# Kernel optimization log

Measured on AMD Instinct MI355X. Metric: run time of the kernel, lower is better.

## Reference

```python
import jax, jax.numpy as jnp
import numpy as np

BUCKET_SIZE = 64
N_HASHES = 8
SELF_ATTN_VALUE = -5e4  # TOKEN_SELF_ATTN_VALUE
EPS = 1e-12  # F.normalize eps


def setup_inputs() -> dict:
    key = jax.random.key(0)
    k1, k2, k3 = jax.random.split(key, 3)
    B, S, D = 16, 4096, 128
    n_buckets = S // BUCKET_SIZE  # 64
    qk = jax.random.normal(k1, (B, S, D), dtype=jnp.float32)
    v = jax.random.normal(k2, (B, S, D), dtype=jnp.float32)
    # rotations_shape = (1, dim, n_hashes, n_buckets // 2); shared across batch
    rotations = jax.random.normal(k3, (1, D, N_HASHES, n_buckets // 2), dtype=jnp.float32)
    return {"qk": qk, "v": v, "rotations": rotations}


def _hash_vectors(qk, rotations, n_buckets):
    # qk: (B,S,D), rotations: (1,D,H,n_buckets//2)
    rotated = jnp.einsum('btf,fhi->bhti', qk, rotations[0])  # (B,H,S,nb/2)
    rotated = jnp.concatenate([rotated, -rotated], axis=-1)   # (B,H,S,nb)
    buckets = jnp.argmax(rotated, axis=-1)                    # (B,H,S)
    offsets = (jnp.arange(N_HASHES) * n_buckets)[None, :, None]
    return (buckets + offsets).reshape(qk.shape[0], -1)       # (B, H*S)


def _look_one_back(x):
    # concat each chunk with its predecessor (circular), along the window dim
    return jnp.concatenate([x, jnp.roll(x, 1, axis=1)], axis=2)


def reference(qk, v, rotations):
    B, S, D = qk.shape
    H = N_HASHES
    n_buckets = S // BUCKET_SIZE
    buckets = _hash_vectors(qk, rotations, n_buckets)         # (B, H*S) int

    ticker = jnp.broadcast_to(jnp.arange(H * S)[None, :], (B, H * S))
    buckets_and_t = S * buckets + (ticker % S)                # unique keys
    sticker = jnp.argsort(buckets_and_t, axis=-1)             # sort by bucket
    undo_sort = jnp.argsort(sticker, axis=-1)

    st = sticker % S                                          # original positions
    sqk = jnp.take_along_axis(qk, st[..., None], axis=1)      # (B,H*S,D)
    sv = jnp.take_along_axis(v, st[..., None], axis=1)

    C = H * n_buckets                                         # num chunks
    bq_t = st.reshape(B, C, -1)                               # (B,C,w)
    bqk = sqk.reshape(B, C, -1, D)
    bv = sv.reshape(B, C, -1, D)
    bq = bqk
    nrm = jnp.maximum(jnp.linalg.norm(bqk, axis=-1, keepdims=True), EPS)
    bk = bqk / nrm                                            # F.normalize

    bk = _look_one_back(bk)                                   # (B,C,2w,D)
    bv = _look_one_back(bv)
    bkv_t = _look_one_back(bq_t)                              # (B,C,2w)

    dots = jnp.einsum('bcie,bcje->bcij', bq, bk) * (D ** -0.5)  # (B,C,w,2w)
    self_mask = bq_t[:, :, :, None] == bkv_t[:, :, None, :]
    dots = jnp.where(self_mask, SELF_ATTN_VALUE, dots)

    lse = jax.scipy.special.logsumexp(dots, axis=-1, keepdims=True)
    probs = jnp.exp(dots - lse)
    bo = jnp.einsum('bcij,bcje->bcie', probs, bv)             # (B,C,w,D)

    so = bo.reshape(B, -1, D)                                 # (B,H*S,D)
    slogits = lse.reshape(B, -1)                              # (B,H*S)
    o = jnp.take_along_axis(so, undo_sort[..., None], axis=1)
    logits = jnp.take_along_axis(slogits, undo_sort, axis=1)

    o = o.reshape(B, H, S, D)
    logits = logits.reshape(B, H, S, 1)
    w = jnp.exp(logits - jax.scipy.special.logsumexp(logits, axis=1, keepdims=True))
    out = jnp.sum(o * w, axis=1)                              # (B,S,D)
    return out
```

## Files before the change

kernel.cpp:

```cpp
#include <hip/hip_runtime.h>
#include <hip/hip_bf16.h>


#define B_ 16
#define S_ 4096
#define D_ 128
#define H_ 8
#define C_ 512
#define L_ 8
#define SCALE_ 0.08838834764831845f

typedef __attribute__((ext_vector_type(8))) short bf16x8;
typedef __attribute__((ext_vector_type(8))) _Float16 f16x8;
typedef __attribute__((ext_vector_type(2))) _Float16 f16x2t;
typedef __attribute__((ext_vector_type(4))) float f32x4;
typedef __attribute__((ext_vector_type(2))) float f32x2v;
typedef __attribute__((ext_vector_type(4))) int int4v;

union BF8U { int4v i; bf16x8 b; };
union F16x8U { int4v i; f16x8 h; };

__device__ __forceinline__ unsigned hi_pack(float x0, float x1) {
    unsigned a, b;
    __builtin_memcpy(&b, &x0, 4);
    __builtin_memcpy(&a, &x1, 4);
    return __builtin_amdgcn_perm(a, b, 0x07060302u);
}
__device__ __forceinline__ float truncbf(float x) {
    unsigned u; __builtin_memcpy(&u, &x, 4);
    u &= 0xFFFF0000u;
    float f; __builtin_memcpy(&f, &u, 4);
    return f;
}
__device__ __forceinline__ unsigned pack2f16(float x0, float x1) {
    f16x2t h = {(_Float16)x0, (_Float16)x1};
    unsigned u; __builtin_memcpy(&u, &h, 4);
    return u;
}
__device__ __forceinline__ unsigned enc_ks(unsigned u) {
    return (u & 0x80000000u) ? ~u : (u | 0x80000000u);
}
__device__ __forceinline__ float dec_ks(unsigned ks) {
    unsigned u = (ks & 0x80000000u) ? (ks ^ 0x80000000u) : ~ks;
    float f; __builtin_memcpy(&f, &u, 4);
    return f;
}

__global__ __launch_bounds__(256) void norm_kernel(const float* __restrict__ qk,
                                                   float* __restrict__ rnrm) {
    int half = threadIdx.x >> 5;
    int lane32 = threadIdx.x & 31;
    size_t row = (size_t)blockIdx.x * 8 + half;
    float4 vv = ((const float4*)(qk + row * D_))[lane32];
    float ss = vv.x * vv.x + vv.y * vv.y + vv.z * vv.z + vv.w * vv.w;
    #pragma unroll
    for (int m = 1; m < 32; m <<= 1) ss += __shfl_xor(ss, m, 64);
    if (lane32 == 0) rnrm[row] = 1.0f / fmaxf(sqrtf(ss), 1e-12f);
}

__global__ __launch_bounds__(256) void prep_rot_kernel(const float* __restrict__ rot,
                                                       short* __restrict__ rth,
                                                       short* __restrict__ rtl) {
    int x = blockIdx.x * 256 + threadIdx.x;
    int hp = x >> 11;
    int ia = (x >> 5) & 63;
    int ft = x & 31;
    float v0 = rot[(size_t)(ft * 4 + 0) * 256 + hp * 64 + ia];
    float v1 = rot[(size_t)(ft * 4 + 1) * 256 + hp * 64 + ia];
    float v2 = rot[(size_t)(ft * 4 + 2) * 256 + hp * 64 + ia];
    float v3 = rot[(size_t)(ft * 4 + 3) * 256 + hp * 64 + ia];
    unsigned h0 = hi_pack(v0, v1), h1 = hi_pack(v2, v3);
    unsigned l0 = hi_pack(v0 - truncbf(v0), v1 - truncbf(v1));
    unsigned l1 = hi_pack(v2 - truncbf(v2), v3 - truncbf(v3));
    int off = ia * 128 + ((((ft >> 1) ^ (ia & 7)) << 3) | ((ft & 1) << 2));
    *(int2*)&rth[hp * 8192 + off] = make_int2((int)h0, (int)h1);
    *(int2*)&rtl[hp * 8192 + off] = make_int2((int)l0, (int)l1);
}

__global__ __launch_bounds__(256, 4) void hash_kernel(
        const float* __restrict__ qk, const float* __restrict__ rot,
        const short* __restrict__ rth, const short* __restrict__ rtl,
        int* __restrict__ buckets) {
    __shared__ unsigned char flags[2][64];

    const int bid = blockIdx.x;
    const int b = bid >> 8;
    const int tile = (bid >> 2) & 63;
    const int hp = bid & 3;
    const int tid = threadIdx.x;
    const int w = tid >> 6, l = tid & 63, g = l >> 4, m = l & 15;

    if (tid < 8) ((int4*)flags)[tid] = make_int4(0, 0, 0, 0);
    __syncthreads();

    const float* qrow = qk + ((size_t)b * S_ + (size_t)tile * 64 + w * 16 + m) * D_;
    bf16x8 qh[4], qlr[4];
    #pragma unroll
    for (int s = 0; s < 4; ++s) {
        float4 xa = *(const float4*)(qrow + s * 32 + g * 8);
        float4 xb = *(const float4*)(qrow + s * 32 + g * 8 + 4);
        BF8U hu, lu;
        hu.i[0] = (int)hi_pack(xa.x, xa.y); hu.i[1] = (int)hi_pack(xa.z, xa.w);
        hu.i[2] = (int)hi_pack(xb.x, xb.y); hu.i[3] = (int)hi_pack(xb.z, xb.w);
        lu.i[0] = (int)hi_pack(xa.x - truncbf(xa.x), xa.y - truncbf(xa.y));
        lu.i[1] = (int)hi_pack(xa.z - truncbf(xa.z), xa.w - truncbf(xa.w));
        lu.i[2] = (int)hi_pack(xb.x - truncbf(xb.x), xb.y - truncbf(xb.y));
        lu.i[3] = (int)hi_pack(xb.z - truncbf(xb.z), xb.w - truncbf(xb.w));
        qh[s] = hu.b; qlr[s] = lu.b;
    }

    f32x4 dots_n[4];
    #pragma unroll
    for (int nt = 0; nt < 4; ++nt) {
        f32x4 acc = (f32x4){0.f, 0.f, 0.f, 0.f};
        #pragma unroll
        for (int s = 0; s < 4; ++s) {
            int kr = hp * 8192 + (nt * 16 + m) * 128 + (((s * 4 + g) ^ (m & 7)) << 3);
            bf16x8 bh = *(const bf16x8*)&rth[kr];
            bf16x8 bl = *(const bf16x8*)&rtl[kr];
            acc = __builtin_amdgcn_mfma_f32_16x16x32_bf16(qh[s], bh, acc, 0, 0, 0);
            acc = __builtin_amdgcn_mfma_f32_16x16x32_bf16(qh[s], bl, acc, 0, 0, 0);
            acc = __builtin_amdgcn_mfma_f32_16x16x32_bf16(qlr[s], bh, acc, 0, 0, 0);
            acc = __builtin_amdgcn_mfma_f32_16x16x32_bf16(qlr[s], bl, acc, 0, 0, 0);
        }
        dots_n[nt] = acc;
    }

    #pragma unroll
    for (int hh = 0; hh < 2; ++hh) {
        int h = hp * 2 + hh;
        #pragma unroll
        for (int r = 0; r < 4; ++r) {
            unsigned long long kM = 0ull, kS = 0ull;
            #pragma unroll
            for (int nn = 0; nn < 2; ++nn) {
                float v = dots_n[hh * 2 + nn][r];
                unsigned u; __builtin_memcpy(&u, &v, 4);
                int i = nn * 16 + m;
                unsigned long long kp =
                    ((unsigned long long)enc_ks(u) << 6) | (unsigned)(63 - i);
                unsigned long long kn =
                    ((unsigned long long)enc_ks(u ^ 0x80000000u) << 6) |
                    (unsigned)(63 - (i + 32));
                if (kp > kM) { kS = kM; kM = kp; } else if (kp > kS) kS = kp;
                if (kn > kM) { kS = kM; kM = kn; } else if (kn > kS) kS = kn;
            }
            #pragma unroll
            for (int st = 1; st <= 8; st <<= 1) {
                unsigned long long oM = __shfl_xor(kM, st, 64);
                unsigned long long oS = __shfl_xor(kS, st, 64);
                unsigned long long lo = kM < oM ? kM : oM;
                kM = kM > oM ? kM : oM;
                unsigned long long hs = kS > oS ? kS : oS;
                kS = hs > lo ? hs : lo;
            }
            if (m == 0) {
                int tok = w * 16 + g * 4 + r;
                int i1 = 63 - (int)(kM & 63ull);
                float v1 = dec_ks((unsigned)(kM >> 6));
                float v2 = dec_ks((unsigned)(kS >> 6));
                if (v1 - v2 < 1e-3f) flags[hh][tok] = 1;
                buckets[(((size_t)(b * H_ + h)) << 12) + tile * 64 + tok] = i1;
            }
        }
    }
    __syncthreads();

    int tok = tid >> 2, part = tid & 3;
    const float* qtok = qk + ((size_t)b * S_ + (size_t)tile * 64 + tok) * D_;
    for (int hh = 0; hh < 2; ++hh) {
        if (!flags[hh][tok]) continue;
        int h = hp * 2 + hh;
        double pd[8] = {0, 0, 0, 0, 0, 0, 0, 0};
        #pragma unroll 2
        for (int f = 0; f < 128; ++f) {
            double q = (double)qtok[f];
            const float* rp = rot + (size_t)f * 256 + h * 32 + part * 8;
            float4 r0 = *(const float4*)rp;
            float4 r1 = *(const float4*)(rp + 4);
            pd[0] = fma(q, (double)r0.x, pd[0]);
            pd[1] = fma(q, (double)r0.y, pd[1]);
            pd[2] = fma(q, (double)r0.z, pd[2]);
            pd[3] = fma(q, (double)r0.w, pd[3]);
            pd[4] = fma(q, (double)r1.x, pd[4]);
            pd[5] = fma(q, (double)r1.y, pd[5]);
            pd[6] = fma(q, (double)r1.z, pd[6]);
            pd[7] = fma(q, (double)r1.w, pd[7]);
        }
        double bv = -1e300; int bi = 0;
        #pragma unroll
        for (int ii = 0; ii < 8; ++ii) {
            int i = part * 8 + ii;
            double v = pd[ii];
            if (v > bv || (v == bv && i < bi)) { bv = v; bi = i; }
            double nv = -v; int ni = i + 32;
            if (nv > bv || (nv == bv && ni < bi)) { bv = nv; bi = ni; }
        }
        #pragma unroll
        for (int mm = 1; mm <= 2; mm <<= 1) {
            double ov = __shfl_xor(bv, mm, 64);
            int oi = __shfl_xor(bi, mm, 64);
            if (ov > bv || (ov == bv && oi < bi)) { bv = ov; bi = oi; }
        }
        if (part == 0)
            buckets[(((size_t)(b * H_ + h)) << 12) + tile * 64 + tok] = bi;
    }
}

__global__ __launch_bounds__(256) void sort_kernel(const int* __restrict__ buckets,
                                                   int* __restrict__ st,
                                                   int* __restrict__ inv,
                                                   const float* __restrict__ rnrm,
                                                   float* __restrict__ rnrm_s) {
    __shared__ unsigned short hist[256][64];
    __shared__ int base[64];
    __shared__ int totals[64];
    int tid = threadIdx.x;
    const int* bkrow = buckets + (size_t)blockIdx.x * S_;
    const float* rnb = rnrm + (size_t)(blockIdx.x >> 3) * S_;

    unsigned int* h32 = (unsigned int*)hist;
    #pragma unroll
    for (int u = 0; u < 32; ++u) h32[u * 256 + tid] = 0;
    __syncthreads();

    #pragma unroll
    for (int u = 0; u < 16; ++u) {
        int t = tid * 16 + u;
        int bk = bkrow[t];
        hist[tid][bk]++;
    }
    __syncthreads();

    if (tid < 64) {
        int bucket = tid;
        int run = 0;
        for (int ch = 0; ch < 256; ++ch) {
            int v = hist[ch][bucket];
            hist[ch][bucket] = (unsigned short)run;
            run += v;
        }
        totals[bucket] = run;
    }
    __syncthreads();
    if (tid == 0) {
        int acc = 0;
        for (int k = 0; k < 64; ++k) { base[k] = acc; acc += totals[k]; }
    }
    __syncthreads();

    int* strow = st + (size_t)blockIdx.x * S_;
    int* invrow = inv + (size_t)blockIdx.x * S_;
    float* rnsrow = rnrm_s + (size_t)blockIdx.x * S_;
    #pragma unroll
    for (int u = 0; u < 16; ++u) {
        int t = tid * 16 + u;
        int bk = bkrow[t];
        int off = hist[tid][bk];
        hist[tid][bk] = (unsigned short)(off + 1);
        int pos = base[bk] + off;
        strow[pos] = t;
        invrow[t] = pos;
        rnsrow[pos] = rnb[t] * SCALE_;
    }
}

__device__ __forceinline__ void transpose4(const float4 v, int g, float (&w_)[4]) {
    bool b0 = (g & 1) != 0, b1 = (g & 2) != 0;
    float k0 = b1 ? v.z : v.x;
    float k1 = b1 ? v.w : v.y;
    float s0 = b1 ? v.x : v.z;
    float s1 = b1 ? v.y : v.w;
    float r0 = __shfl_xor(s0, 32, 64);
    float r1 = __shfl_xor(s1, 32, 64);
    float kq_ = b0 ? k1 : k0;
    float rq_ = b0 ? r1 : r0;
    float sk  = b0 ? k0 : k1;
    float sr  = b0 ? r0 : r1;
    float tk_ = __shfl_xor(sk, 16, 64);
    float tr_ = __shfl_xor(sr, 16, 64);
    float A0 = b0 ? tk_ : kq_;
    float A1 = b0 ? kq_ : tk_;
    float B0 = b0 ? tr_ : rq_;
    float B1 = b0 ? rq_ : tr_;
    w_[0] = b1 ? B0 : A0;
    w_[1] = b1 ? B1 : A1;
    w_[2] = b1 ? A0 : B0;
    w_[3] = b1 ? A1 : B1;
}

template<bool DENSE>
__global__ __launch_bounds__(256, 2) void attn_strip_kernel(
        const float* __restrict__ qk, const float* __restrict__ rnrm_s,
        const float* __restrict__ vglob, const int* __restrict__ st,
        float* __restrict__ outnum, float* __restrict__ den,
        _Float16* __restrict__ snum, float* __restrict__ sden) {
    __shared__ int   toks[2][64];
    __shared__ float rnss[2][64];
    __shared__ short kbuf[2][8192];
    __shared__ short vbuf[2][8192];

    const int p = blockIdx.x;
    const int lg = (p & 7) * 128 + (p >> 3);
    const int b = lg >> 6;
    const int strip = lg & 63;
    const int c0 = strip * L_;
    const int tid = threadIdx.x;
    const int w = tid >> 6, l = tid & 63, g = l >> 4, m = l & 15;
    const size_t bS = ((size_t)b << 12);
    const int* stb = st + ((size_t)b << 15);

    auto rns_base = [&](int c) -> size_t {
        return (((size_t)(b * H_ + (c >> 6))) << 12) + (size_t)(c & 63) * 64;
    };

    float4 kreg[8];
    float4 va[4], vb[4];

    auto issue_k = [&](const int* __restrict__ tk) {
        #pragma unroll
        for (int u = 0; u < 8; ++u) {
            int token = u * 8 + (tid >> 5);
            int cc = tid & 31;
            kreg[u] = *(const float4*)(qk + (bS + tk[token]) * D_ + cc * 4);
        }
    };
    auto write_k = [&](short* __restrict__ kb) {
        #pragma unroll
        for (int u = 0; u < 8; ++u) {
            int token = u * 8 + (tid >> 5);
            int cc = tid & 31;
            float4 vv = kreg[u];
            unsigned h0 = pack2f16(vv.x, vv.y), h1 = pack2f16(vv.z, vv.w);
            int kw = token * 128 + ((((cc >> 1) ^ (token & 7)) << 3) | ((cc & 1) << 2));
            *(int2*)&kb[kw] = make_int2((int)h0, (int)h1);
        }
    };
    auto issue_v = [&](const int* __restrict__ tk) {
        #pragma unroll
        for (int up = 0; up < 4; ++up) {
            int kq8 = w * 16 + (up & 1) * 8;
            int cc = (up >> 1) * 16 + m;
            va[up] = *(const float4*)(vglob + (bS + tk[kq8 + g]) * D_ + cc * 4);
            vb[up] = *(const float4*)(vglob + (bS + tk[kq8 + 4 + g]) * D_ + cc * 4);
        }
    };
    auto write_v = [&](short* __restrict__ vq) {
        #pragma unroll
        for (int up = 0; up < 4; ++up) {
            int kq8 = w * 16 + (up & 1) * 8;
            int cc = (up >> 1) * 16 + m;
            float wa[4], wb[4];
            transpose4(va[up], g, wa);
            transpose4(vb[up], g, wb);
            unsigned h0 = pack2f16(wa[0], wa[1]), h1 = pack2f16(wa[2], wa[3]);
            unsigned h2 = pack2f16(wb[0], wb[1]), h3 = pack2f16(wb[2], wb[3]);
            int d = cc * 4 + g;
            int ds = d ^ ((d >> 3) & 7);
            int kg = kq8 >> 3;
            int idx = (kg * 128 + ds) * 8;
            *(int4*)&vq[idx] = make_int4((int)h0, (int)h1, (int)h2, (int)h3);
        }
    };

    const int cprev = (c0 + 511) & 511;
    if (tid < 64) {
        toks[1][tid] = stb[cprev * 64 + tid];
        rnss[1][tid] = rnrm_s[rns_base(cprev) + tid];
        toks[0][tid] = stb[c0 * 64 + tid];
        rnss[0][tid] = rnrm_s[rns_base(c0) + tid];
    }
    __syncthreads();
    issue_k(toks[1]);
    issue_v(toks[1]);
    write_k(kbuf[1]);
    write_v(vbuf[1]);
    __syncthreads();
    issue_k(toks[0]);

    #pragma unroll 1
    for (int j = 0; j < L_; ++j) {
        const int c = c0 + j;
        const int cur = j & 1, prv = cur ^ 1;
        short* kbc = kbuf[cur];
        short* kbp = kbuf[prv];
        short* vbc = vbuf[cur];
        short* vbp = vbuf[prv];

        write_k(kbc);
        __syncthreads();

        f16x8 qh[4];
        #pragma unroll
        for (int s4 = 0; s4 < 4; ++s4) {
            int qr = (w * 16 + m) * 128 + (((s4 * 4 + g) ^ (m & 7)) << 3);
            qh[s4] = *(const f16x8*)&kbc[qr];
        }
        const int qtok_m = toks[cur][w * 16 + m];
        issue_v(toks[cur]);

        f32x4 e4s[4], e4p[4];
        float densum = 0.f;
        auto qk_one = [&](const short* __restrict__ kb,
                          const float* __restrict__ rns,
                          const int* __restrict__ tkp, int mode,
                          f32x4 (&e4)[4]) {
            #pragma unroll
            for (int kt = 0; kt < 4; ++kt) {
                f32x4 acc = (f32x4){0.f, 0.f, 0.f, 0.f};
                #pragma unroll
                for (int s4 = 0; s4 < 4; ++s4) {
                    int kr = (kt * 16 + m) * 128 + (((s4 * 4 + g) ^ (m & 7)) << 3);
                    f16x8 ah = *(const f16x8*)&kb[kr];
                    acc = __builtin_amdgcn_mfma_f32_16x16x32_f16(ah, qh[s4], acc, 0, 0, 0);
                }
                f32x4 rn4 = *(const f32x4*)&rns[kt * 16 + g * 4];
                int4v kt4;
                if (mode == 1) kt4 = *(const int4v*)&tkp[kt * 16 + g * 4];
                f32x4 e;
                #pragma unroll
                for (int r = 0; r < 4; ++r) {
                    float ev = __expf(acc[r] * rn4[r]);
                    if (mode == 0) {
                        if (kt == w && (g * 4 + r) == m) ev = 0.0f;
                    } else {
                        if (kt4[r] == qtok_m) ev = 0.0f;
                    }
                    e[r] = ev;
                    densum += ev;
                }
                e4[kt] = e;
            }
        };
        qk_one(kbc, rnss[cur], toks[cur], 0, e4s);
        qk_one(kbp, rnss[prv], toks[prv], 1, e4p);
        __syncthreads();

        if (j + 1 < L_ && tid < 64) {
            int cn = c + 1;
            toks[prv][tid] = stb[cn * 64 + tid];
            rnss[prv][tid] = rnrm_s[rns_base(cn) + tid];
        }
        write_v(vbc);
        __syncthreads();

        if (j + 1 < L_) issue_k(toks[prv]);

        f32x4 acc_o[8];
        #pragma unroll
        for (int dt = 0; dt < 8; ++dt) acc_o[dt] = (f32x4){0.f, 0.f, 0.f, 0.f};
        auto pv_one = [&](const short* __restrict__ vq, const f32x4 (&e4)[4]) {
            #pragma unroll
            for (int s = 0; s < 2; ++s) {
                float pav[8];
                #pragma unroll
                for (int c2 = 0; c2 < 2; ++c2) {
                    int srcLane = ((g & 1) * 2 + c2) * 16 + m;
                    #pragma unroll
                    for (int r = 0; r < 4; ++r) {
                        float v0 = __shfl(e4[2 * s][r], srcLane, 64);
                        float v1 = __shfl(e4[2 * s + 1][r], srcLane, 64);
                        pav[c2 * 4 + r] = (g >> 1) ? v1 : v0;
                    }
                }
                F16x8U pahu;
                #pragma unroll
                for (int j2 = 0; j2 < 4; ++j2)
                    pahu.i[j2] = (int)pack2f16(pav[2 * j2], pav[2 * j2 + 1]);
                f16x8 pah = pahu.h;
                #pragma unroll
                for (int dt = 0; dt < 8; ++dt) {
                    int d = dt * 16 + m;
                    int ds = d ^ ((d >> 3) & 7);
                    int base = ((s * 4 + g) * 128 + ds) * 8;
                    f16x8 vh = *(const f16x8*)&vq[base];
                    acc_o[dt] = __builtin_amdgcn_mfma_f32_16x16x32_f16(pah, vh, acc_o[dt], 0, 0, 0);
                }
            }
        };
        pv_one(vbc, e4s);
        pv_one(vbp, e4p);

        densum += __shfl_xor(densum, 16, 64);
        densum += __shfl_xor(densum, 32, 64);

        if (DENSE) {
            const int h = c >> 6;
            const size_t base = (((size_t)(b * H_ + h)) << 12) + (size_t)(c & 63) * 64;
            #pragma unroll
            for (int r = 0; r < 4; ++r) {
                int row = w * 16 + g * 4 + r;
                _Float16* nrow = snum + (base + row) * D_;
                #pragma unroll
                for (int dt = 0; dt < 8; ++dt)
                    __builtin_nontemporal_store((_Float16)acc_o[dt][r], nrow + dt * 16 + m);
            }
            if (g == 0) __builtin_nontemporal_store(densum, sden + base + w * 16 + m);
        } else {
            if (g == 0) atomicAdd(den + bS + qtok_m, densum);
            int4v q4tok = *(const int4v*)&toks[cur][w * 16 + g * 4];
            #pragma unroll
            for (int r = 0; r < 4; ++r) {
                float* obase = outnum + ((bS + q4tok[r]) * D_);
                #pragma unroll
                for (int dt = 0; dt < 8; ++dt)
                    atomicAdd(obase + dt * 16 + m, acc_o[dt][r]);
            }
        }
    }
}

__global__ __launch_bounds__(256) void combine_kernel(
        const _Float16* __restrict__ snum, const float* __restrict__ sden,
        const int* __restrict__ inv, float* __restrict__ out) {
    int wv = threadIdx.x >> 6, l = threadIdx.x & 63;
    int t = blockIdx.x * 4 + wv;
    int b = t >> 12, s = t & 4095;
    float s0 = 0.f, s1 = 0.f, dsum = 0.f;
    #pragma unroll
    for (int h = 0; h < H_; ++h) {
        int bh = b * H_ + h;
        int pos = inv[((size_t)bh << 12) + s];
        size_t row = ((size_t)bh << 12) + pos;
        dsum += __builtin_nontemporal_load(sden + row);
        unsigned uv = __builtin_nontemporal_load(
            (const unsigned*)(snum + row * D_ + 2 * l));
        unsigned short us0 = (unsigned short)(uv & 0xFFFFu);
        unsigned short us1 = (unsigned short)(uv >> 16);
        _Float16 h0, h1;
        __builtin_memcpy(&h0, &us0, 2);
        __builtin_memcpy(&h1, &us1, 2);
        s0 += (float)h0;
        s1 += (float)h1;
    }
    float rd = 1.0f / dsum;
    f32x2v o2 = {s0 * rd, s1 * rd};
    __builtin_nontemporal_store(o2, (f32x2v*)(out + (size_t)t * D_ + 2 * l));
}

__global__ __launch_bounds__(256) void div_kernel(float* __restrict__ out,
                                                  const float* __restrict__ den) {
    int i = blockIdx.x * 256 + threadIdx.x;
    float4 o = ((float4*)out)[i];
    float dn = den[i >> 5];
    ((float4*)out)[i] = make_float4(o.x / dn, o.y / dn, o.z / dn, o.w / dn);
}

extern "C" void kernel_launch(void* const* d_in, const int* in_sizes, int n_in,
                              void* d_out, int out_size, void* d_ws, size_t ws_size,
                              hipStream_t stream) {
    const float* qk  = (const float*)d_in[0];
    const float* v   = (const float*)d_in[1];
    const float* rot = (const float*)d_in[2];
    float* out = (float*)d_out;

    char* ws = (char*)d_ws;
    float* rnrm    = (float*)ws;
    int* buckets   = (int*)(ws + 262144);
    int* inv       = buckets;
    int* st        = (int*)(ws + 2359296);
    float* rnrm_s  = (float*)(ws + 4456448);
    float* sden    = (float*)(ws + 6553600);
    short* rth     = (short*)(ws + 8650752);
    short* rtl     = (short*)(ws + 8716288);
    _Float16* snum = (_Float16*)(ws + 8781824);
    const size_t need = 8781824ull + 134217728ull;

    norm_kernel<<<B_ * S_ / 8, 256, 0, stream>>>(qk, rnrm);
    prep_rot_kernel<<<32, 256, 0, stream>>>(rot, rth, rtl);
    hash_kernel<<<B_ * (S_ / 64) * 4, 256, 0, stream>>>(qk, rot, rth, rtl, buckets);
    sort_kernel<<<B_ * H_, 256, 0, stream>>>(buckets, st, inv, rnrm, rnrm_s);

    if (ws_size >= need) {
        attn_strip_kernel<true><<<B_ * C_ / L_, 256, 0, stream>>>(
            qk, rnrm_s, v, st, nullptr, nullptr, snum, sden);
        combine_kernel<<<B_ * S_ / 4, 256, 0, stream>>>(snum, sden, inv, out);
    } else {
        float* den = sden;
        hipMemsetAsync(out, 0, (size_t)B_ * S_ * D_ * 4, stream);
        hipMemsetAsync(den, 0, (size_t)B_ * S_ * 4, stream);
        attn_strip_kernel<false><<<B_ * C_ / L_, 256, 0, stream>>>(
            qk, rnrm_s, v, st, out, den, nullptr, nullptr);
        div_kernel<<<B_ * S_ * D_ / 4 / 256, 256, 0, stream>>>(out, den);
    }
}
```

Before: 223.4 us.

## Single-buffer V in LDS, raise occupancy, and pack snum stores with permuted layout

Measured after the change: 342.9 us. +53.5%, slower.

```diff
diff --git a/kernel.cpp b/kernel.cpp
--- a/kernel.cpp
+++ b/kernel.cpp
@@ -14,7 +14,6 @@
 typedef __attribute__((ext_vector_type(8))) _Float16 f16x8;
 typedef __attribute__((ext_vector_type(2))) _Float16 f16x2t;
 typedef __attribute__((ext_vector_type(4))) float f32x4;
-typedef __attribute__((ext_vector_type(2))) float f32x2v;
 typedef __attribute__((ext_vector_type(4))) int int4v;
 
 union BF8U { int4v i; bf16x8 b; };
@@ -290,7 +289,7 @@
 }
 
 template<bool DENSE>
-__global__ __launch_bounds__(256, 2) void attn_strip_kernel(
+__global__ __launch_bounds__(256, 3) void attn_strip_kernel(
         const float* __restrict__ qk, const float* __restrict__ rnrm_s,
         const float* __restrict__ vglob, const int* __restrict__ st,
         float* __restrict__ outnum, float* __restrict__ den,
@@ -298,7 +297,7 @@
     __shared__ int   toks[2][64];
     __shared__ float rnss[2][64];
     __shared__ short kbuf[2][8192];
-    __shared__ short vbuf[2][8192];
+    __shared__ short vbuf[8192];
 
     const int p = blockIdx.x;
     const int lg = (p & 7) * 128 + (p >> 3);
@@ -345,7 +344,7 @@
             vb[up] = *(const float4*)(vglob + (bS + tk[kq8 + 4 + g]) * D_ + cc * 4);
         }
     };
-    auto write_v = [&](short* __restrict__ vq) {
+    auto write_v = [&]() {
         #pragma unroll
         for (int up = 0; up < 4; ++up) {
             int kq8 = w * 16 + (up & 1) * 8;
@@ -359,7 +358,7 @@
             int ds = d ^ ((d >> 3) & 7);
             int kg = kq8 >> 3;
             int idx = (kg * 128 + ds) * 8;
-            *(int4*)&vq[idx] = make_int4((int)h0, (int)h1, (int)h2, (int)h3);
+            *(int4*)&vbuf[idx] = make_int4((int)h0, (int)h1, (int)h2, (int)h3);
         }
     };
 
@@ -374,7 +373,7 @@
     issue_k(toks[1]);
     issue_v(toks[1]);
     write_k(kbuf[1]);
-    write_v(vbuf[1]);
+    write_v();
     __syncthreads();
     issue_k(toks[0]);
 
@@ -384,8 +383,6 @@
         const int cur = j & 1, prv = cur ^ 1;
         short* kbc = kbuf[cur];
         short* kbp = kbuf[prv];
-        short* vbc = vbuf[cur];
-        short* vbp = vbuf[prv];
 
         write_k(kbc);
         __syncthreads();
@@ -434,22 +431,11 @@
         };
         qk_one(kbc, rnss[cur], toks[cur], 0, e4s);
         qk_one(kbp, rnss[prv], toks[prv], 1, e4p);
-        __syncthreads();
-
-        if (j + 1 < L_ && tid < 64) {
-            int cn = c + 1;
-            toks[prv][tid] = stb[cn * 64 + tid];
-            rnss[prv][tid] = rnrm_s[rns_base(cn) + tid];
-        }
-        write_v(vbc);
-        __syncthreads();
-
-        if (j + 1 < L_) issue_k(toks[prv]);
 
         f32x4 acc_o[8];
         #pragma unroll
         for (int dt = 0; dt < 8; ++dt) acc_o[dt] = (f32x4){0.f, 0.f, 0.f, 0.f};
-        auto pv_one = [&](const short* __restrict__ vq, const f32x4 (&e4)[4]) {
+        auto pv_one = [&](const f32x4 (&e4)[4]) {
             #pragma unroll
             for (int s = 0; s < 2; ++s) {
                 float pav[8];
@@ -473,29 +459,44 @@
                     int d = dt * 16 + m;
                     int ds = d ^ ((d >> 3) & 7);
                     int base = ((s * 4 + g) * 128 + ds) * 8;
-                    f16x8 vh = *(const f16x8*)&vq[base];
+                    f16x8 vh = *(const f16x8*)&vbuf[base];
                     acc_o[dt] = __builtin_amdgcn_mfma_f32_16x16x32_f16(pah, vh, acc_o[dt], 0, 0, 0);
                 }
             }
         };
-        pv_one(vbc, e4s);
-        pv_one(vbp, e4p);
+        pv_one(e4p);
+        __syncthreads();
+
+        if (j + 1 < L_ && tid < 64) {
+            int cn = c + 1;
+            toks[prv][tid] = stb[cn * 64 + tid];
+            rnss[prv][tid] = rnrm_s[rns_base(cn) + tid];
+        }
+        write_v();
+        __syncthreads();
+
+        if (j + 1 < L_) issue_k(toks[prv]);
+
+        pv_one(e4s);
 
         densum += __shfl_xor(densum, 16, 64);
         densum += __shfl_xor(densum, 32, 64);
 
         if (DENSE) {
-            const int h = c >> 6;
-            const size_t base = (((size_t)(b * H_ + h)) << 12) + (size_t)(c & 63) * 64;
+            const int hH = c >> 6;
+            const size_t basepos = (((size_t)(b * H_ + hH)) << 12) + (size_t)(c & 63) * 64;
             #pragma unroll
             for (int r = 0; r < 4; ++r) {
                 int row = w * 16 + g * 4 + r;
-                _Float16* nrow = snum + (base + row) * D_;
-                #pragma unroll
-                for (int dt = 0; dt < 8; ++dt)
-                    __builtin_nontemporal_store((_Float16)acc_o[dt][r], nrow + dt * 16 + m);
-            }
-            if (g == 0) __builtin_nontemporal_store(densum, sden + base + w * 16 + m);
+                int4v pk;
+                pk[0] = (int)pack2f16(acc_o[0][r], acc_o[1][r]);
+                pk[1] = (int)pack2f16(acc_o[2][r], acc_o[3][r]);
+                pk[2] = (int)pack2f16(acc_o[4][r], acc_o[5][r]);
+                pk[3] = (int)pack2f16(acc_o[6][r], acc_o[7][r]);
+                __builtin_nontemporal_store(
+                    pk, (int4v*)(snum + (basepos + row) * D_ + m * 8));
+            }
+            if (g == 0) __builtin_nontemporal_store(densum, sden + basepos + w * 16 + m);
         } else {
             if (g == 0) atomicAdd(den + bS + qtok_m, densum);
             int4v q4tok = *(const int4v*)&toks[cur][w * 16 + g * 4];
@@ -534,8 +535,9 @@
         s1 += (float)h1;
     }
     float rd = 1.0f / dsum;
-    f32x2v o2 = {s0 * rd, s1 * rd};
-    __builtin_nontemporal_store(o2, (f32x2v*)(out + (size_t)t * D_ + 2 * l));
+    int d0 = ((2 * l) & 7) * 16 + (l >> 2);
+    __builtin_nontemporal_store(s0 * rd, out + (size_t)t * D_ + d0);
+    __builtin_nontemporal_store(s1 * rd, out + (size_t)t * D_ + d0 + 16);
 }
 
 __global__ __launch_bounds__(256) void div_kernel(float* __restrict__ out,
```
